# Kernel tuning notes

Measured on AMD Instinct MI355X. Metric: run time of the kernel, lower is better.

The kernel has to match this reference:

```python
import jax, jax.numpy as jnp
import numpy as np

MANUAL_PAD = 3
PAD = (2, 1)        # zero pad inside upfirdn2d (pad0, pad1)
UP_CROP = 0
UPSAMPLE_FACTOR = 1


def _make_kernel():
    # make_kernel([1,3,3,1]): outer product, normalized to sum 1
    k = jnp.array([1.0, 3.0, 3.0, 1.0], dtype=jnp.float32)
    k = k[None, :] * k[:, None]
    k = k / k.sum()
    if UPSAMPLE_FACTOR > 1:
        k = k * (UPSAMPLE_FACTOR ** 2)
    return k


def setup_inputs() -> dict:
    key = jax.random.key(0)
    x = jax.random.normal(key, (4, 512, 256, 256), dtype=jnp.float32)
    return {"input": x, "kernel": _make_kernel()}


def reference(input, kernel):
    mp = MANUAL_PAD
    # circular pad by manual_pad on both spatial dims
    x = jnp.pad(input, ((0, 0), (0, 0), (mp, mp), (mp, mp)), mode="wrap")
    # upfirdn2d with up=down=1, pad=(pad0, pad1): zero pad then FIR conv
    x = jnp.pad(x, ((0, 0), (0, 0), (PAD[0], PAD[1]), (PAD[0], PAD[1])))
    C = x.shape[1]
    # torch upfirdn2d_native flips the kernel before conv2d (true convolution)
    w = jnp.flip(kernel, (0, 1))[None, None].astype(x.dtype)  # [1,1,kh,kw]
    w = jnp.tile(w, (C, 1, 1, 1))                              # depthwise [C,1,kh,kw]
    out = jax.lax.conv_general_dilated(
        x, w,
        window_strides=(1, 1),
        padding="VALID",
        dimension_numbers=("NCHW", "OIHW", "NCHW"),
        feature_group_count=C,
    )
    h, wd = out.shape[2], out.shape[3]
    if UP_CROP != 0:
        out = out[:, :, 2 * UP_CROP:h - 2 * UP_CROP, 2 * UP_CROP:wd - 2 * UP_CROP]
    else:
        out = out[:, :, mp:h - mp, mp:wd - mp]
    return out
```

## Files before the change

kernel.cpp:

```cpp
#include <hip/hip_runtime.h>


#define IMG 256

__global__ __launch_bounds__(256) void circular_blur_kernel(
    const float* __restrict__ in, float* __restrict__ out, int n_img)
{
    const int img = blockIdx.x;
    if (img >= n_img) return;
    const float* __restrict__ src = in + (size_t)img * IMG * IMG;
    float* __restrict__ dst = out + (size_t)img * IMG * IMG;

    const int t  = threadIdx.x;
    const int lr = t >> 6;
    const int lc = (t & 63) << 2;

    __shared__ float buf[2][4][IMG];

    const int cm2 = (t + 254) & 255;
    const int cm1 = (t + 255) & 255;
    const int cp1 = (t + 1)   & 255;

    {
        const int r = 252 + lr;
        *reinterpret_cast<float4*>(&buf[0][lr][lc]) =
            *reinterpret_cast<const float4*>(src + r * IMG + lc);
    }
    __syncthreads();

    float hm3, hm2, hm1;
    {
        float a, b, c, d;
        a = buf[0][1][cm2]; b = buf[0][1][cm1]; c = buf[0][1][t]; d = buf[0][1][cp1];
        hm3 = (a + d + 3.0f * (b + c)) * 0.125f;
        a = buf[0][2][cm2]; b = buf[0][2][cm1]; c = buf[0][2][t]; d = buf[0][2][cp1];
        hm2 = (a + d + 3.0f * (b + c)) * 0.125f;
        a = buf[0][3][cm2]; b = buf[0][3][cm1]; c = buf[0][3][t]; d = buf[0][3][cp1];
        hm1 = (a + d + 3.0f * (b + c)) * 0.125f;
    }

    int pb = 1;
    for (int ch = 0; ch < 64; ++ch) {
        const int r0 = ch << 2;
        {
            const int r = r0 + lr;
            *reinterpret_cast<float4*>(&buf[pb][lr][lc]) =
                *reinterpret_cast<const float4*>(src + r * IMG + lc);
        }
        __syncthreads();

        float h0, h1, h2, h3;
        {
            float a, b, c, d;
            a = buf[pb][0][cm2]; b = buf[pb][0][cm1]; c = buf[pb][0][t]; d = buf[pb][0][cp1];
            h0 = (a + d + 3.0f * (b + c)) * 0.125f;
            a = buf[pb][1][cm2]; b = buf[pb][1][cm1]; c = buf[pb][1][t]; d = buf[pb][1][cp1];
            h1 = (a + d + 3.0f * (b + c)) * 0.125f;
            a = buf[pb][2][cm2]; b = buf[pb][2][cm1]; c = buf[pb][2][t]; d = buf[pb][2][cp1];
            h2 = (a + d + 3.0f * (b + c)) * 0.125f;
            a = buf[pb][3][cm2]; b = buf[pb][3][cm1]; c = buf[pb][3][t]; d = buf[pb][3][cp1];
            h3 = (a + d + 3.0f * (b + c)) * 0.125f;
        }

        dst[(size_t)((r0 - 1) & 255) * IMG + t] = (hm3 + h0 + 3.0f * (hm2 + hm1)) * 0.125f;
        dst[(size_t)(r0    ) * IMG + t]         = (hm2 + h1 + 3.0f * (hm1 + h0)) * 0.125f;
        dst[(size_t)(r0 + 1) * IMG + t]         = (hm1 + h2 + 3.0f * (h0  + h1)) * 0.125f;
        dst[(size_t)(r0 + 2) * IMG + t]         = (h0  + h3 + 3.0f * (h1  + h2)) * 0.125f;

        hm3 = h1; hm2 = h2; hm1 = h3;
        pb ^= 1;
    }
}

extern "C" void kernel_launch(void* const* d_in, const int* in_sizes, int n_in,
                              void* d_out, int out_size, void* d_ws, size_t ws_size,
                              hipStream_t stream) {
    const float* in = (const float*)d_in[0];
    float* out = (float*)d_out;
    const int n_img = in_sizes[0] / (IMG * IMG);
    circular_blur_kernel<<<n_img, 256, 0, stream>>>(in, out, n_img);
}
```

Measured before the change: 225.1 us.

## Replace shared-memory row staging with wave shuffles and per-wave row strips

Each 64-lane wave now owns a 64-row strip of the image. It loads a full row as float4 per lane and does the horizontal 4-tap filter with cross-lane shuffles instead of LDS staging. This removes the per-row-chunk __syncthreads and the shared-memory traffic, and turns the scalar stores into float4 stores. The cost is three redundant halo rows per wave and a loop that is serial per wave, with less load parallelism in flight per iteration.

Measured after the change: 220.1 us. 2.2% less time.

```diff
diff --git a/kernel.cpp b/kernel.cpp
--- a/kernel.cpp
+++ b/kernel.cpp
@@ -3,72 +3,58 @@
 
 #define IMG 256
 
+__device__ __forceinline__ float4 hrow(const float4 v, int lm1, int lp1) {
+    const float zm = __shfl(v.z, lm1, 64);
+    const float wm = __shfl(v.w, lm1, 64);
+    const float xp = __shfl(v.x, lp1, 64);
+    float4 h;
+    h.x = (zm  + v.y) + 3.0f * (wm  + v.x);
+    h.y = (wm  + v.z) + 3.0f * (v.x + v.y);
+    h.z = (v.x + v.w) + 3.0f * (v.y + v.z);
+    h.w = (v.y + xp ) + 3.0f * (v.z + v.w);
+    return h;
+}
+
 __global__ __launch_bounds__(256) void circular_blur_kernel(
-    const float* __restrict__ in, float* __restrict__ out, int n_img)
+    const float* __restrict__ in, float* __restrict__ out)
 {
-    const int img = blockIdx.x;
-    if (img >= n_img) return;
-    const float* __restrict__ src = in + (size_t)img * IMG * IMG;
-    float* __restrict__ dst = out + (size_t)img * IMG * IMG;
+    const int img  = blockIdx.x;
+    const int lane = threadIdx.x & 63;
+    const int wid  = threadIdx.x >> 6;
+    const int R0   = wid << 6;
 
-    const int t  = threadIdx.x;
-    const int lr = t >> 6;
-    const int lc = (t & 63) << 2;
+    const float* __restrict__ src = in  + (size_t)img * IMG * IMG + (lane << 2);
+    float*       __restrict__ dst = out + (size_t)img * IMG * IMG + (lane << 2);
 
-    __shared__ float buf[2][4][IMG];
+    const int lm1 = (lane + 63) & 63;
+    const int lp1 = (lane + 1)  & 63;
 
-    const int cm2 = (t + 254) & 255;
-    const int cm1 = (t + 255) & 255;
-    const int cp1 = (t + 1)   & 255;
-
+    float4 hm3, hm2, hm1;
     {
-        const int r = 252 + lr;
-        *reinterpret_cast<float4*>(&buf[0][lr][lc]) =
-            *reinterpret_cast<const float4*>(src + r * IMG + lc);
-    }
-    __syncthreads();
-
-    float hm3, hm2, hm1;
-    {
-        float a, b, c, d;
-        a = buf[0][1][cm2]; b = buf[0][1][cm1]; c = buf[0][1][t]; d = buf[0][1][cp1];
-        hm3 = (a + d + 3.0f * (b + c)) * 0.125f;
-        a = buf[0][2][cm2]; b = buf[0][2][cm1]; c = buf[0][2][t]; d = buf[0][2][cp1];
-        hm2 = (a + d + 3.0f * (b + c)) * 0.125f;
-        a = buf[0][3][cm2]; b = buf[0][3][cm1]; c = buf[0][3][t]; d = buf[0][3][cp1];
-        hm1 = (a + d + 3.0f * (b + c)) * 0.125f;
+        float4 v;
+        v = *reinterpret_cast<const float4*>(src + (size_t)((R0 + 254) & 255) * IMG);
+        hm3 = hrow(v, lm1, lp1);
+        v = *reinterpret_cast<const float4*>(src + (size_t)((R0 + 255) & 255) * IMG);
+        hm2 = hrow(v, lm1, lp1);
+        v = *reinterpret_cast<const float4*>(src + (size_t)R0 * IMG);
+        hm1 = hrow(v, lm1, lp1);
     }
 
-    int pb = 1;
-    for (int ch = 0; ch < 64; ++ch) {
-        const int r0 = ch << 2;
-        {
-            const int r = r0 + lr;
-            *reinterpret_cast<float4*>(&buf[pb][lr][lc]) =
-                *reinterpret_cast<const float4*>(src + r * IMG + lc);
-        }
-        __syncthreads();
+    #pragma unroll 4
+    for (int i = 0; i < 64; ++i) {
+        const int rl = (R0 + 1 + i) & 255;
+        const float4 v = *reinterpret_cast<const float4*>(src + (size_t)rl * IMG);
+        const float4 h = hrow(v, lm1, lp1);
 
-        float h0, h1, h2, h3;
-        {
-            float a, b, c, d;
-            a = buf[pb][0][cm2]; b = buf[pb][0][cm1]; c = buf[pb][0][t]; d = buf[pb][0][cp1];
-            h0 = (a + d + 3.0f * (b + c)) * 0.125f;
-            a = buf[pb][1][cm2]; b = buf[pb][1][cm1]; c = buf[pb][1][t]; d = buf[pb][1][cp1];
-            h1 = (a + d + 3.0f * (b + c)) * 0.125f;
-            a = buf[pb][2][cm2]; b = buf[pb][2][cm1]; c = buf[pb][2][t]; d = buf[pb][2][cp1];
-            h2 = (a + d + 3.0f * (b + c)) * 0.125f;
-            a = buf[pb][3][cm2]; b = buf[pb][3][cm1]; c = buf[pb][3][t]; d = buf[pb][3][cp1];
-            h3 = (a + d + 3.0f * (b + c)) * 0.125f;
-        }
+        const float s = 0.015625f;
+        float4 o;
+        o.x = ((hm3.x + h.x) + 3.0f * (hm2.x + hm1.x)) * s;
+        o.y = ((hm3.y + h.y) + 3.0f * (hm2.y + hm1.y)) * s;
+        o.z = ((hm3.z + h.z) + 3.0f * (hm2.z + hm1.z)) * s;
+        o.w = ((hm3.w + h.w) + 3.0f * (hm2.w + hm1.w)) * s;
+        *reinterpret_cast<float4*>(dst + (size_t)(R0 + i) * IMG) = o;
 
-        dst[(size_t)((r0 - 1) & 255) * IMG + t] = (hm3 + h0 + 3.0f * (hm2 + hm1)) * 0.125f;
-        dst[(size_t)(r0    ) * IMG + t]         = (hm2 + h1 + 3.0f * (hm1 + h0)) * 0.125f;
-        dst[(size_t)(r0 + 1) * IMG + t]         = (hm1 + h2 + 3.0f * (h0  + h1)) * 0.125f;
-        dst[(size_t)(r0 + 2) * IMG + t]         = (h0  + h3 + 3.0f * (h1  + h2)) * 0.125f;
-
-        hm3 = h1; hm2 = h2; hm1 = h3;
-        pb ^= 1;
+        hm3 = hm2; hm2 = hm1; hm1 = h;
     }
 }
 
@@ -78,5 +64,5 @@
     const float* in = (const float*)d_in[0];
     float* out = (float*)d_out;
     const int n_img = in_sizes[0] / (IMG * IMG);
-    circular_blur_kernel<<<n_img, 256, 0, stream>>>(in, out, n_img);
+    circular_blur_kernel<<<n_img, 256, 0, stream>>>(in, out);
 }
```
